# Kernel optimization log

Hardware: AMD Instinct MI355X
Metric: run time of the kernel (lower is better)

## Reference

```python
import jax, jax.numpy as jnp
import numpy as np

N = 80000      # nodes (spots)
D = 1000       # input_dim (genes)
E = 1280000    # edges (avg degree 16)
FH1, FH2 = 64, 16
GH1, GH2 = 64, 16
K = 10         # dec_cluster_n
ALPHA = 1.0
MASK = int(0.8 * N)
BN_EPS = 1e-3


def _xavier(key, shape):
    fan_in, fan_out = shape[0], shape[1]
    lim = jnp.sqrt(6.0 / (fan_in + fan_out))
    return jax.random.uniform(key, shape, jnp.float32, -lim, lim)


def setup_inputs() -> dict:
    key = jax.random.key(0)
    ks = jax.random.split(key, 32)
    x = jax.random.normal(ks[0], (N, D), jnp.float32)
    edge_rows = jax.random.randint(ks[1], (E,), 0, N, jnp.int32)
    edge_cols = jax.random.randint(ks[2], (E,), 0, N, jnp.int32)
    edge_vals = jax.random.uniform(ks[3], (E,), jnp.float32)
    mask_nodes = jax.random.permutation(ks[4], N)[:MASK].astype(jnp.int32)
    enc_mask_token = 0.02 * jax.random.normal(ks[5], (1, D), jnp.float32)
    # encoder L1: Linear + BatchNorm (eval: running stats)
    W1 = _xavier(ks[6], (D, FH1)); b1 = jnp.zeros((FH1,), jnp.float32)
    g1 = jnp.ones((FH1,), jnp.float32); be1 = jnp.zeros((FH1,), jnp.float32)
    rm1 = 0.1 * jax.random.normal(ks[7], (FH1,), jnp.float32)
    rv1 = 0.5 + jax.random.uniform(ks[8], (FH1,), jnp.float32)
    # encoder L2
    W2 = _xavier(ks[9], (FH1, FH2)); b2 = jnp.zeros((FH2,), jnp.float32)
    g2 = jnp.ones((FH2,), jnp.float32); be2 = jnp.zeros((FH2,), jnp.float32)
    rm2 = 0.1 * jax.random.normal(ks[10], (FH2,), jnp.float32)
    rv2 = 0.5 + jax.random.uniform(ks[11], (FH2,), jnp.float32)
    # GCN weights
    Wgc1 = _xavier(ks[12], (FH2, GH1))
    Wgc2 = _xavier(ks[13], (GH1, GH2))
    Wgc3 = _xavier(ks[14], (GH1, GH2))
    Wdec = _xavier(ks[15], (GH2 + FH2, D))
    cluster_layer = jax.random.normal(ks[16], (K, GH2 + FH2), jnp.float32) * jnp.sqrt(2.0 / (K + GH2 + FH2))
    return dict(x=x, edge_rows=edge_rows, edge_cols=edge_cols, edge_vals=edge_vals,
                mask_nodes=mask_nodes, enc_mask_token=enc_mask_token,
                W1=W1, b1=b1, g1=g1, be1=be1, rm1=rm1, rv1=rv1,
                W2=W2, b2=b2, g2=g2, be2=be2, rm2=rm2, rv2=rv2,
                Wgc1=Wgc1, Wgc2=Wgc2, Wgc3=Wgc3, Wdec=Wdec,
                cluster_layer=cluster_layer)


def _bn_eval(h, g, b, rm, rv):
    return (h - rm) * (g * jax.lax.rsqrt(rv + BN_EPS)) + b


def _spmm(rows, cols, vals, dense):
    # sparse adj [N,N] @ dense [N,F]
    return jax.ops.segment_sum(vals[:, None] * dense[cols], rows, num_segments=N)


def _l2norm(v):
    n = jnp.sqrt(jnp.sum(v * v, axis=-1, keepdims=True))
    return v / jnp.maximum(n, 1e-12)


def reference(x, edge_rows, edge_cols, edge_vals, mask_nodes, enc_mask_token,
              W1, b1, g1, be1, rm1, rv1, W2, b2, g2, be2, rm2, rv2,
              Wgc1, Wgc2, Wgc3, Wdec, cluster_layer):
    # encoding_mask_noise: add mask token to masked nodes (eval: dropout off)
    out_x = x.at[mask_nodes].add(enc_mask_token[0])
    # dense encoder (Linear -> BN(eval) -> ELU; dropout off)
    h = jax.nn.elu(_bn_eval(out_x @ W1 + b1, g1, be1, rm1, rv1))
    feat_x = jax.nn.elu(_bn_eval(h @ W2 + b2, g2, be2, rm2, rv2))
    # GCN layers: mm then spmm
    hidden1 = jax.nn.relu(_spmm(edge_rows, edge_cols, edge_vals, feat_x @ Wgc1))
    mu = _spmm(edge_rows, edge_cols, edge_vals, hidden1 @ Wgc2)
    logvar = _spmm(edge_rows, edge_cols, edge_vals, hidden1 @ Wgc3)
    gnn_z = mu  # eval-mode reparameterize
    z = jnp.concatenate([feat_x, gnn_z], axis=1)  # [N, 32]
    de_feat = _spmm(edge_rows, edge_cols, edge_vals, z @ Wdec)  # identity act
    # student-t cluster soft assignments
    d2 = jnp.sum(jnp.square(z[:, None, :] - cluster_layer[None, :, :]), axis=2)  # [N,K]
    q = 1.0 / (1.0 + d2 / ALPHA)
    q = q ** ((ALPHA + 1.0) / 2.0)
    q = q / jnp.sum(q, axis=1, keepdims=True)
    # sce loss on masked nodes
    x_init = out_x[mask_nodes]
    x_rec = de_feat[mask_nodes]
    loss = jnp.mean((1.0 - jnp.sum(_l2norm(x_rec) * _l2norm(x_init), axis=-1)) ** 3)
    return (z, mu, logvar, de_feat, q, feat_x, gnn_z, loss)
```

## Files before the change

kernel.cpp:

```cpp
#include <hip/hip_runtime.h>
#include <hip/hip_bf16.h>
#include <math.h>

#define Nn 80000
#define Dd 1000
#define Ee 1280000
#define MM 64000
#define NT 32

typedef __attribute__((ext_vector_type(8))) short bf16x8;
typedef __attribute__((ext_vector_type(4))) float f32x4;

__device__ inline unsigned short f2bf(float f){
  union { float f; unsigned u; } c; c.f = f;
  unsigned u = c.u;
  u += 0x7FFFu + ((u >> 16) & 1u);
  return (unsigned short)(u >> 16);
}
__device__ inline float bf2f(unsigned short s){
  return __uint_as_float(((unsigned)s) << 16);
}

__device__ __forceinline__ void gload16(const void* g, void* l){
  __builtin_amdgcn_global_load_lds(
      (const __attribute__((address_space(1))) void*)g,
      (__attribute__((address_space(3))) void*)l, 16, 0, 0);
}

__device__ __forceinline__ bf16x8 cvt8(f32x4 a, f32x4 b){
  union { __hip_bfloat162 h; unsigned u; } c0, c1, c2, c3;
  c0.h = __float22bfloat162_rn(make_float2(a.x, a.y));
  c1.h = __float22bfloat162_rn(make_float2(a.z, a.w));
  c2.h = __float22bfloat162_rn(make_float2(b.x, b.y));
  c3.h = __float22bfloat162_rn(make_float2(b.z, b.w));
  union { unsigned u[4]; bf16x8 v; } r;
  r.u[0] = c0.u; r.u[1] = c1.u; r.u[2] = c2.u; r.u[3] = c3.u;
  return r.v;
}

__global__ __launch_bounds__(256) void k_init(const float* __restrict__ W1,
    const float* __restrict__ Wdec, const float* __restrict__ token,
    unsigned short* __restrict__ Wim, unsigned short* __restrict__ WdT2,
    float* __restrict__ tw, int* __restrict__ flags, int* __restrict__ deg,
    float* __restrict__ loss)
{
  int i = blockIdx.x*256 + threadIdx.x;
  if (i < 131072){
    int t   = i >> 12;
    int rem = i & 4095;
    int c   = rem >> 5;
    int pos = rem & 31;
    int slot = pos >> 3;
    int j    = pos & 7;
    int u    = slot ^ (c & 3);
    int k    = t*32 + u*8 + j;
    float v = 0.f;
    if (c < 96 && k < Dd) v = (c < 64) ? W1[k*64 + c] : Wdec[(size_t)(c-64)*Dd + k];
    Wim[i] = f2bf(v);
  }
  unsigned t1 = (unsigned)(i - 131072);
  if (t1 < 32768u){
    int col = t1 >> 5, k = t1 & 31;
    WdT2[t1] = (col < Dd) ? f2bf(Wdec[(size_t)k*Dd + col]) : (unsigned short)0;
  }
  if (i < Nn){ flags[i] = 0; deg[i] = 0; }
  if (i == 0) *loss = 0.f;
  unsigned u3 = (unsigned)(i - 163840);
  if (u3 < 6208u){
    int j = u3 >> 6, l = u3 & 63;
    float s = 0.f;
    if (j < 64){ for (int k = l; k < Dd; k += 64) s += token[k]*W1[k*64 + j]; }
    else if (j < 96){ const float* wr = Wdec + (size_t)(j-64)*Dd;
                      for (int k = l; k < Dd; k += 64) s += token[k]*wr[k]; }
    else { for (int k = l; k < Dd; k += 64) s += token[k]*token[k]; }
    #pragma unroll
    for (int o = 32; o; o >>= 1) s += __shfl_down(s, o);
    if (l == 0) tw[j] = s;
  }
}

__global__ __launch_bounds__(256) void k_flags(const int* __restrict__ mask,
    int* __restrict__ flags)
{
  int i = blockIdx.x*256 + threadIdx.x;
  if (i < MM) flags[mask[i]] = 1;
}

__global__ __launch_bounds__(256, 3) void k_gemm1(
    const float* __restrict__ x, const unsigned short* __restrict__ Wim,
    const int* __restrict__ flags, const float* __restrict__ tw,
    const float* __restrict__ token,
    const float* __restrict__ b1, const float* __restrict__ g1,
    const float* __restrict__ be1, const float* __restrict__ rm1,
    const float* __restrict__ rv1, const float* __restrict__ W2,
    const float* __restrict__ b2, const float* __restrict__ g2,
    const float* __restrict__ be2, const float* __restrict__ rm2,
    const float* __restrict__ rv2, float* __restrict__ fx,
    float* __restrict__ wx, float* __restrict__ sii_node,
    const int* __restrict__ erow, const int* __restrict__ ecol,
    const float* __restrict__ evls, int* __restrict__ deg,
    int2* __restrict__ buck)
{
  __shared__ char smem[53248];
  if (blockIdx.x >= 625){
    int i = (blockIdx.x - 625)*256 + threadIdx.x;
    if (i < Ee){
      int r = erow[i];
      int s = atomicAdd(&deg[r], 1);
      if (s < 64){
        int2 pr; pr.x = ecol[i]; pr.y = __float_as_int(evls[i]);
        buck[((size_t)r << 6) + s] = pr;
      }
    }
    return;
  }
  float* tokL = (float*)(smem + 49152);
  const int tid  = threadIdx.x;
  const int lane = tid & 63;
  const int wave = tid >> 6;
  const int wm = wave >> 1, wn = wave & 1;
  const int l15 = lane & 15, kg = lane >> 4;
  const int swz = l15 & 7;
  const int row0 = blockIdx.x * 128;

  for (int i = tid; i < 1024; i += 256) tokL[i] = (i < Dd) ? token[i] : 0.f;
  __syncthreads();

  auto stage = [&](int t, char* Ab, char* Bb){
    int k0 = t*32;
    #pragma unroll
    for (int j = 0; j < 4; ++j){
      int s = (wave*4 + j)*64 + lane;
      int r = s >> 3, u = s & 7;
      int col = k0 + ((u ^ (r & 7)) << 2);
      if (col > 996) col = 996;
      gload16(x + (size_t)(row0 + r)*Dd + col, Ab + (wave*4 + j)*1024);
    }
    const char* wim = (const char*)Wim + (size_t)t*8192;
    #pragma unroll
    for (int j = 0; j < 2; ++j){
      int ch = wave*2 + j;
      gload16(wim + ch*1024 + lane*16, Bb + ch*1024);
    }
  };

  stage(0, smem,         smem + 32768);
  stage(1, smem + 16384, smem + 40960);

  const f32x4 zero4 = {0.f,0.f,0.f,0.f};
  f32x4 acc[4][3];
  #pragma unroll
  for (int i = 0; i < 4; ++i){ acc[i][0]=zero4; acc[i][1]=zero4; acc[i][2]=zero4; }
  float sx2[4] = {0.f,0.f,0.f,0.f};
  float sxt[4] = {0.f,0.f,0.f,0.f};

  #pragma unroll 2
  for (int t = 0; t < NT; ++t){
    if (t < NT-1) asm volatile("s_waitcnt vmcnt(6)" ::: "memory");
    else          asm volatile("s_waitcnt vmcnt(0)" ::: "memory");
    __builtin_amdgcn_s_barrier();
    __builtin_amdgcn_sched_barrier(0);

    const char* Ab = smem + (t&1)*16384;
    const char* Bb = smem + 32768 + (t&1)*8192;
    const int k0 = t*32;

    f32x4 tk0 = *(const f32x4*)(tokL + k0 + kg*8);
    f32x4 tk1 = *(const f32x4*)(tokL + k0 + kg*8 + 4);

    bf16x8 bfr[3];
    #pragma unroll
    for (int ni = 0; ni < 3; ++ni){
      int c = wn*48 + ni*16 + l15;
      bfr[ni] = *(const bf16x8*)(Bb + c*64 + ((kg ^ (c & 3)) << 4));
    }
    bool kv = (k0 + kg*8) <= 992;
    #pragma unroll
    for (int mi = 0; mi < 4; ++mi){
      int r = wm*64 + mi*16 + l15;
      f32x4 xa = *(const f32x4*)(Ab + r*128 + (((2*kg  ) ^ swz) << 4));
      f32x4 xb = *(const f32x4*)(Ab + r*128 + (((2*kg+1) ^ swz) << 4));
      if (wn == 0 && kv){
        sx2[mi] += xa.x*xa.x + xa.y*xa.y + xa.z*xa.z + xa.w*xa.w
                 + xb.x*xb.x + xb.y*xb.y + xb.z*xb.z + xb.w*xb.w;
        sxt[mi] += xa.x*tk0.x + xa.y*tk0.y + xa.z*tk0.z + xa.w*tk0.w
                 + xb.x*tk1.x + xb.y*tk1.y + xb.z*tk1.z + xb.w*tk1.w;
      }
      bf16x8 af = cvt8(xa, xb);
      acc[mi][0] = __builtin_amdgcn_mfma_f32_16x16x32_bf16(af, bfr[0], acc[mi][0], 0, 0, 0);
      acc[mi][1] = __builtin_amdgcn_mfma_f32_16x16x32_bf16(af, bfr[1], acc[mi][1], 0, 0, 0);
      acc[mi][2] = __builtin_amdgcn_mfma_f32_16x16x32_bf16(af, bfr[2], acc[mi][2], 0, 0, 0);
    }

    __builtin_amdgcn_sched_barrier(0);
    __builtin_amdgcn_s_barrier();
    if (t + 2 < NT)
      stage(t+2, smem + (t&1)*16384, smem + 32768 + (t&1)*8192);
  }

  float stt = tw[96];
  if (wn == 0){
    #pragma unroll
    for (int mi = 0; mi < 4; ++mi){
      float a2 = sx2[mi]; a2 += __shfl_xor(a2, 16); a2 += __shfl_xor(a2, 32);
      float at = sxt[mi]; at += __shfl_xor(at, 16); at += __shfl_xor(at, 32);
      if (lane < 16){
        int row = row0 + wm*64 + mi*16 + lane;
        float fl = flags[row] ? 1.f : 0.f;
        sii_node[row] = a2 + fl*(2.f*at + stt);
      }
    }
  }

  float flv[4][4];
  #pragma unroll
  for (int mi = 0; mi < 4; ++mi)
    #pragma unroll
    for (int r4 = 0; r4 < 4; ++r4)
      flv[mi][r4] = flags[row0 + wm*64 + mi*16 + (lane>>4)*4 + r4] ? 1.f : 0.f;

  float* Hs  = (float*)smem;
  float* W2s = (float*)(smem + 36864);
  for (int i = tid; i < 1024; i += 256) W2s[i] = W2[i];

  #pragma unroll
  for (int ni = 0; ni < 3; ++ni){
    int n = wn*48 + ni*16 + l15;
    float twn = tw[n];
    if (n < 64){
      float bb = b1[n], rmv = rm1[n];
      float scv = g1[n]*rsqrtf(rv1[n] + 1e-3f), bev = be1[n];
      #pragma unroll
      for (int mi = 0; mi < 4; ++mi){
        #pragma unroll
        for (int r4 = 0; r4 < 4; ++r4){
          int lrow = wm*64 + mi*16 + (lane>>4)*4 + r4;
          float v = (acc[mi][ni][r4] + flv[mi][r4]*twn + bb - rmv)*scv + bev;
          v = (v > 0.f) ? v : expm1f(v);
          Hs[lrow*66 + n] = v;
        }
      }
    } else {
      int j = n - 64;
      #pragma unroll
      for (int mi = 0; mi < 4; ++mi){
        #pragma unroll
        for (int r4 = 0; r4 < 4; ++r4){
          int lrow = wm*64 + mi*16 + (lane>>4)*4 + r4;
          wx[(size_t)(row0 + lrow)*32 + j] = acc[mi][ni][r4] + flv[mi][r4]*twn;
        }
      }
    }
  }
  __syncthreads();

  {
    int j = tid & 15;
    float pb = b2[j], prm = rm2[j];
    float psc = g2[j]*rsqrtf(rv2[j] + 1e-3f), pbe = be2[j];
    int rb = (tid >> 4) * 8;
    #pragma unroll
    for (int rr = 0; rr < 8; ++rr){
      int r = rb + rr;
      float a = pb;
      #pragma unroll
      for (int k = 0; k < 64; ++k) a += Hs[r*66 + k]*W2s[k*16 + j];
      float v = (a - prm)*psc + pbe;
      v = (v > 0.f) ? v : expm1f(v);
      fx[(size_t)(row0 + r)*16 + j] = v;
    }
  }
}

__global__ __launch_bounds__(256) void k_spmm16(const int* __restrict__ deg,
    const int2* __restrict__ buck, const float* __restrict__ in,
    float* __restrict__ out, const float* __restrict__ Wgc1,
    unsigned short* __restrict__ h1b)
{
  __shared__ float Ws[1024];
  for (int t = threadIdx.x; t < 1024; t += 256) Ws[t] = Wgc1[t];
  __syncthreads();
  int row = blockIdx.x*16 + (threadIdx.x >> 4);
  int l = threadIdx.x & 15;
  int d = deg[row]; if (d > 64) d = 64;
  const int2* bp = buck + ((size_t)row << 6);
  float acc = 0.f;
  for (int p = 0; p < d; ++p){
    int2 ce = bp[p];
    acc += __int_as_float(ce.y) * in[(size_t)ce.x*16 + l];
  }
  out[(size_t)row*16 + l] = acc;
  float h0=0.f, h1=0.f, h2=0.f, h3=0.f;
  #pragma unroll
  for (int k = 0; k < 16; ++k){
    float av = __shfl(acc, k, 16);
    const float* wp = &Ws[k*64 + l*4];
    h0 += av*wp[0]; h1 += av*wp[1]; h2 += av*wp[2]; h3 += av*wp[3];
  }
  ushort4 pk;
  pk.x = f2bf(fmaxf(h0, 0.f)); pk.y = f2bf(fmaxf(h1, 0.f));
  pk.z = f2bf(fmaxf(h2, 0.f)); pk.w = f2bf(fmaxf(h3, 0.f));
  *reinterpret_cast<ushort4*>(&h1b[(size_t)row*64 + l*4]) = pk;
}

__global__ __launch_bounds__(256) void k_gcn2(const int* __restrict__ deg,
    const int2* __restrict__ buck, const unsigned short* __restrict__ h1b,
    const float* __restrict__ Wgc2, const float* __restrict__ Wgc3,
    const float* __restrict__ fx, const float* __restrict__ cl,
    float* __restrict__ z, float* __restrict__ mu,
    float* __restrict__ lv, float* __restrict__ gz, float* __restrict__ q)
{
  __shared__ float ah[16][65];
  __shared__ float Ws[2048];
  __shared__ float cls[320];
  __shared__ float zs[16][33];
  __shared__ float qv[16][10];
  int t = threadIdx.x;
  for (int i = t; i < 1024; i += 256){ Ws[i] = Wgc2[i]; Ws[1024 + i] = Wgc3[i]; }
  for (int i = t; i < 320; i += 256) cls[i] = cl[i];
  const int wave = t >> 6, lane = t & 63;
  const int row0 = blockIdx.x*16;
  #pragma unroll
  for (int rr = 0; rr < 4; ++rr){
    int lr = wave*4 + rr;
    int row = row0 + lr;
    int d = deg[row]; if (d > 64) d = 64;
    const int2* bp = buck + ((size_t)row << 6);
    float acc = 0.f;
    for (int p = 0; p < d; ++p){
      int2 ce = bp[p];
      acc += __int_as_float(ce.y) * bf2f(h1b[(size_t)ce.x*64 + lane]);
    }
    ah[lr][lane] = acc;
  }
  __syncthreads();
  {
    int r = t >> 4, j = t & 15;
    const float* ar = ah[r];
    float m = 0.f, l = 0.f;
    #pragma unroll 16
    for (int k = 0; k < 64; ++k){
      float a = ar[k];
      m += a*Ws[k*16 + j];
      l += a*Ws[1024 + k*16 + j];
    }
    size_t grow = (size_t)(row0 + r);
    mu[grow*16 + j] = m;
    gz[grow*16 + j] = m;
    z[grow*32 + 16 + j] = m;
    zs[r][16 + j] = m;
    lv[grow*16 + j] = l;
    float v = fx[grow*16 + j];
    z[grow*32 + j] = v;
    zs[r][j] = v;
  }
  __syncthreads();
  if (t < 160){
    int r = t / 10, c = t - r*10;
    float d2 = 0.f;
    #pragma unroll
    for (int k = 0; k < 32; ++k){ float d = zs[r][k] - cls[c*32 + k]; d2 += d*d; }
    qv[r][c] = 1.f/(1.f + d2);
  }
  __syncthreads();
  if (t < 160){
    int r = t / 10, c = t - r*10;
    float ss = 0.f;
    #pragma unroll
    for (int cc = 0; cc < 10; ++cc) ss += qv[r][cc];
    q[(size_t)(row0 + r)*10 + c] = qv[r][c]/ss;
  }
}

__global__ __launch_bounds__(256) void k_dec(const float* __restrict__ afx,
    const float* __restrict__ mu, const int* __restrict__ deg,
    const int2* __restrict__ buck, const unsigned short* __restrict__ WdT2,
    const float* __restrict__ wx, const float* __restrict__ sii_node,
    const int* __restrict__ flags, float* __restrict__ de,
    float* __restrict__ loss)
{
  __shared__ float stg[4][16][68];
  __shared__ float amuL[64][17];
  __shared__ float bsum[4];
  const int tid  = threadIdx.x;
  const int lane = tid & 63;
  const int wave = tid >> 6;
  const int base = blockIdx.x*64;

  {
    int l = tid & 15, rg = tid >> 4;
    #pragma unroll
    for (int pass = 0; pass < 4; ++pass){
      int lr = pass*16 + rg;
      int row = base + lr;
      int d = deg[row]; if (d > 64) d = 64;
      const int2* bp = buck + ((size_t)row << 6);
      float acc = 0.f;
      for (int p = 0; p < d; ++p){
        int2 ce = bp[p];
        acc += __int_as_float(ce.y) * mu[(size_t)ce.x*16 + l];
      }
      amuL[lr][l] = acc;
    }
  }
  __syncthreads();

  const int r0 = base + wave*16;
  const int kg = lane >> 4;
  const int l15 = lane & 15;
  const int row = r0 + l15;
  f32x4 a0, a1;
  if (kg < 2){
    const float* asrc = afx + (size_t)row*16 + kg*8;
    a0 = *reinterpret_cast<const f32x4*>(asrc);
    a1 = *reinterpret_cast<const f32x4*>(asrc + 4);
  } else {
    const float* asrc = &amuL[wave*16 + l15][(kg-2)*8];
    a0 = *reinterpret_cast<const f32x4*>(asrc);
    a1 = *reinterpret_cast<const f32x4*>(asrc + 4);
  }
  bf16x8 af = cvt8(a0, a1);
  const float* wsrc = wx + (size_t)row*32 + kg*8;
  f32x4 w0 = *reinterpret_cast<const f32x4*>(wsrc);
  f32x4 w1 = *reinterpret_cast<const f32x4*>(wsrc + 4);
  float sri = a0.x*w0.x + a0.y*w0.y + a0.z*w0.z + a0.w*w0.w
            + a1.x*w1.x + a1.y*w1.y + a1.z*w1.z + a1.w*w1.w;

  const f32x4 zero4 = {0.f,0.f,0.f,0.f};
  float sq = 0.f;
  float (*S)[68] = stg[wave];
  const int srow = lane >> 4;
  const int scol = l15*4;

  for (int g = 0; g < 16; ++g){
    int c0 = g*64;
    #pragma unroll
    for (int j = 0; j < 4; ++j){
      int cb = c0 + j*16;
      bf16x8 bf = *reinterpret_cast<const bf16x8*>(&WdT2[(size_t)(cb + l15)*32 + kg*8]);
      f32x4 d = __builtin_amdgcn_mfma_f32_16x16x32_bf16(bf, af, zero4, 0, 0, 0);
      sq += d[0]*d[0] + d[1]*d[1] + d[2]*d[2] + d[3]*d[3];
      *reinterpret_cast<f32x4*>(&S[l15][j*16 + kg*4]) = d;
    }
    asm volatile("s_waitcnt lgkmcnt(0)" ::: "memory");
    __builtin_amdgcn_sched_barrier(0);
    #pragma unroll
    for (int sub = 0; sub < 4; ++sub){
      int lr = sub*4 + srow;
      int cc = c0 + scol;
      if (cc < Dd){
        f32x4 v = *reinterpret_cast<const f32x4*>(&S[lr][scol]);
        *reinterpret_cast<f32x4*>(&de[(size_t)(r0 + lr)*Dd + cc]) = v;
      }
    }
    __builtin_amdgcn_sched_barrier(0);
    asm volatile("s_waitcnt lgkmcnt(0)" ::: "memory");
  }
  sq  += __shfl_xor(sq, 16);  sq  += __shfl_xor(sq, 32);
  sri += __shfl_xor(sri, 16); sri += __shfl_xor(sri, 32);
  float tval = 0.f;
  if (kg == 0){
    float nr = fmaxf(sqrtf(sq), 1e-12f);
    float ni = fmaxf(sqrtf(sii_node[row]), 1e-12f);
    float tt = 1.f - sri/(nr*ni);
    tval = flags[row] ? tt*tt*tt : 0.f;
  }
  #pragma unroll
  for (int o = 1; o < 16; o <<= 1) tval += __shfl_xor(tval, o);
  if (lane == 0) bsum[wave] = tval;
  __syncthreads();
  if (tid == 0)
    atomicAdd(loss, (bsum[0] + bsum[1] + bsum[2] + bsum[3]) * (1.f/MM));
}

extern "C" void kernel_launch(void* const* d_in, const int* in_sizes, int n_in,
                              void* d_out, int out_size, void* d_ws, size_t ws_size,
                              hipStream_t stream)
{
  const float* x     = (const float*)d_in[0];
  const int*   erow  = (const int*)  d_in[1];
  const int*   ecol  = (const int*)  d_in[2];
  const float* evls  = (const float*)d_in[3];
  const int*   mask  = (const int*)  d_in[4];
  const float* token = (const float*)d_in[5];
  const float* W1  = (const float*)d_in[6];
  const float* b1  = (const float*)d_in[7];
  const float* g1  = (const float*)d_in[8];
  const float* be1 = (const float*)d_in[9];
  const float* rm1 = (const float*)d_in[10];
  const float* rv1 = (const float*)d_in[11];
  const float* W2  = (const float*)d_in[12];
  const float* b2  = (const float*)d_in[13];
  const float* g2  = (const float*)d_in[14];
  const float* be2 = (const float*)d_in[15];
  const float* rm2 = (const float*)d_in[16];
  const float* rv2 = (const float*)d_in[17];
  const float* Wgc1= (const float*)d_in[18];
  const float* Wgc2= (const float*)d_in[19];
  const float* Wgc3= (const float*)d_in[20];
  const float* Wdec= (const float*)d_in[21];
  const float* clus= (const float*)d_in[22];

  float* out = (float*)d_out;
  float* oz  = out;
  float* omu = out + (size_t)Nn*32;
  float* olv = omu + (size_t)Nn*16;
  float* ode = olv + (size_t)Nn*16;
  float* oq  = ode + (size_t)Nn*1000;
  float* ofx = oq  + (size_t)Nn*10;
  float* ogz = ofx + (size_t)Nn*16;
  float* olo = ogz + (size_t)Nn*16;

  char* w = (char*)d_ws;
  unsigned short* Wim  = (unsigned short*)w; w += (size_t)262144;
  unsigned short* WdT2 = (unsigned short*)w; w += (size_t)65536;
  float* tw    = (float*)w; w += 512;
  int* flags   = (int*)w;   w += (size_t)Nn*4;
  int* deg     = (int*)w;   w += (size_t)Nn*4;
  int2* buck   = (int2*)w;  w += (size_t)Nn*64*8;
  float* afx   = (float*)w; w += (size_t)Nn*16*4;
  unsigned short* h1b = (unsigned short*)w; w += (size_t)Nn*64*2;
  float* wx    = (float*)w; w += (size_t)Nn*32*4;
  float* sii   = (float*)w; w += (size_t)Nn*4;

  k_init<<<dim3(665), dim3(256), 0, stream>>>(W1, Wdec, token, Wim, WdT2, tw,
      flags, deg, olo);
  k_flags<<<dim3((MM+255)/256), dim3(256), 0, stream>>>(mask, flags);
  k_gemm1<<<dim3(5625), dim3(256), 0, stream>>>(x, Wim, flags, tw, token,
      b1, g1, be1, rm1, rv1, W2, b2, g2, be2, rm2, rv2, ofx, wx, sii,
      erow, ecol, evls, deg, buck);
  k_spmm16<<<dim3(Nn/16), dim3(256), 0, stream>>>(deg, buck, ofx, afx, Wgc1, h1b);
  k_gcn2<<<dim3(Nn/16), dim3(256), 0, stream>>>(deg, buck, h1b, Wgc2, Wgc3,
      ofx, clus, oz, omu, olv, ogz, oq);
  k_dec<<<dim3(Nn/64), dim3(256), 0, stream>>>(afx, omu, deg, buck, WdT2,
      wx, sii, flags, ode, olo);
}
```

Baseline: 489.7 us.

## Stage x through registers as bf16 in LDS to shrink shared memory for occupancy

After: 485.8 us, median of 2. No clear change (-0.8%).

```diff
diff --git a/kernel.cpp b/kernel.cpp
--- a/kernel.cpp
+++ b/kernel.cpp
@@ -86,7 +86,7 @@
   if (i < MM) flags[mask[i]] = 1;
 }
 
-__global__ __launch_bounds__(256, 3) void k_gemm1(
+__global__ __launch_bounds__(256, 4) void k_gemm1(
     const float* __restrict__ x, const unsigned short* __restrict__ Wim,
     const int* __restrict__ flags, const float* __restrict__ tw,
     const float* __restrict__ token,
@@ -101,7 +101,7 @@
     const float* __restrict__ evls, int* __restrict__ deg,
     int2* __restrict__ buck)
 {
-  __shared__ char smem[53248];
+  __shared__ char smem[37888];
   if (blockIdx.x >= 625){
     int i = (blockIdx.x - 625)*256 + threadIdx.x;
     if (i < Ee){
@@ -114,38 +114,36 @@
     }
     return;
   }
-  float* tokL = (float*)(smem + 49152);
+  unsigned short* As = (unsigned short*)smem;
+  float* tokL = (float*)(smem + 24576);
   const int tid  = threadIdx.x;
   const int lane = tid & 63;
   const int wave = tid >> 6;
   const int wm = wave >> 1, wn = wave & 1;
   const int l15 = lane & 15, kg = lane >> 4;
-  const int swz = l15 & 7;
   const int row0 = blockIdx.x * 128;
 
+  const int rtid = tid >> 3;
+  const int kq   = (tid & 7) * 4;
+  const int wu   = (kq >> 3) ^ (rtid & 3) ^ ((rtid >> 2) & 3);
+  const int wofs = rtid*32 + wu*8 + (kq & 4);
+
+  const float* xbase = x + (size_t)row0 * Dd;
+  f32x4 ra[4];
+
   for (int i = tid; i < 1024; i += 256) tokL[i] = (i < Dd) ? token[i] : 0.f;
-  __syncthreads();
-
-  auto stage = [&](int t, char* Ab, char* Bb){
-    int k0 = t*32;
-    #pragma unroll
-    for (int j = 0; j < 4; ++j){
-      int s = (wave*4 + j)*64 + lane;
-      int r = s >> 3, u = s & 7;
-      int col = k0 + ((u ^ (r & 7)) << 2);
-      if (col > 996) col = 996;
-      gload16(x + (size_t)(row0 + r)*Dd + col, Ab + (wave*4 + j)*1024);
-    }
-    const char* wim = (const char*)Wim + (size_t)t*8192;
-    #pragma unroll
-    for (int j = 0; j < 2; ++j){
-      int ch = wave*2 + j;
-      gload16(wim + ch*1024 + lane*16, Bb + ch*1024);
-    }
-  };
-
-  stage(0, smem,         smem + 32768);
-  stage(1, smem + 16384, smem + 40960);
+
+  {
+    int col = kq;
+    #pragma unroll
+    for (int j = 0; j < 4; ++j)
+      ra[j] = *(const f32x4*)(xbase + (size_t)(j*32 + rtid)*Dd + col);
+    const char* wim = (const char*)Wim;
+    gload16(wim + (wave*2  )*1024 + lane*16, smem + 8192 + (wave*2  )*1024);
+    gload16(wim + (wave*2+1)*1024 + lane*16, smem + 8192 + (wave*2+1)*1024);
+  }
+  asm volatile("s_waitcnt lgkmcnt(0)" ::: "memory");
+  __builtin_amdgcn_s_barrier();
 
   const f32x4 zero4 = {0.f,0.f,0.f,0.f};
   f32x4 acc[4][3];
@@ -156,17 +154,42 @@
 
   #pragma unroll 2
   for (int t = 0; t < NT; ++t){
-    if (t < NT-1) asm volatile("s_waitcnt vmcnt(6)" ::: "memory");
-    else          asm volatile("s_waitcnt vmcnt(0)" ::: "memory");
+    const char* Bb = smem + 8192 + (t&1)*8192;
+    const int k0 = t*32;
+    const bool kok = (t < NT-1) || (kq <= 4);
+    f32x4 tok4 = *(const f32x4*)(tokL + k0 + kq);
+
+    #pragma unroll
+    for (int j = 0; j < 4; ++j){
+      f32x4 v = ra[j];
+      if (kok){
+        sx2[j] += v.x*v.x + v.y*v.y + v.z*v.z + v.w*v.w;
+        sxt[j] += v.x*tok4.x + v.y*tok4.y + v.z*tok4.z + v.w*tok4.w;
+      }
+      union { __hip_bfloat162 h; unsigned u; } c0, c1;
+      c0.h = __float22bfloat162_rn(make_float2(v.x, v.y));
+      c1.h = __float22bfloat162_rn(make_float2(v.z, v.w));
+      uint2 pk; pk.x = c0.u; pk.y = c1.u;
+      *reinterpret_cast<uint2*>(&As[j*1024 + wofs]) = pk;
+    }
+
+    if (t + 1 < NT){
+      int col = k0 + 32 + kq; if (col > 996) col = 996;
+      #pragma unroll
+      for (int j = 0; j < 4; ++j)
+        ra[j] = *(const f32x4*)(xbase + (size_t)(j*32 + rtid)*Dd + col);
+      const char* wim = (const char*)Wim + (size_t)(t+1)*8192;
+      char* Bn = smem + 8192 + ((t+1)&1)*8192;
+      gload16(wim + (wave*2  )*1024 + lane*16, Bn + (wave*2  )*1024);
+      gload16(wim + (wave*2+1)*1024 + lane*16, Bn + (wave*2+1)*1024);
+      asm volatile("s_waitcnt lgkmcnt(0)" ::: "memory");
+      asm volatile("s_waitcnt vmcnt(6)" ::: "memory");
+    } else {
+      asm volatile("s_waitcnt lgkmcnt(0)" ::: "memory");
+      asm volatile("s_waitcnt vmcnt(0)" ::: "memory");
+    }
     __builtin_amdgcn_s_barrier();
     __builtin_amdgcn_sched_barrier(0);
-
-    const char* Ab = smem + (t&1)*16384;
-    const char* Bb = smem + 32768 + (t&1)*8192;
-    const int k0 = t*32;
-
-    f32x4 tk0 = *(const f32x4*)(tokL + k0 + kg*8);
-    f32x4 tk1 = *(const f32x4*)(tokL + k0 + kg*8 + 4);
 
     bf16x8 bfr[3];
     #pragma unroll
@@ -174,41 +197,30 @@
       int c = wn*48 + ni*16 + l15;
       bfr[ni] = *(const bf16x8*)(Bb + c*64 + ((kg ^ (c & 3)) << 4));
     }
-    bool kv = (k0 + kg*8) <= 992;
+    const int ru = (kg ^ (l15 & 3) ^ ((l15 >> 2) & 3)) << 4;
     #pragma unroll
     for (int mi = 0; mi < 4; ++mi){
       int r = wm*64 + mi*16 + l15;
-      f32x4 xa = *(const f32x4*)(Ab + r*128 + (((2*kg  ) ^ swz) << 4));
-      f32x4 xb = *(const f32x4*)(Ab + r*128 + (((2*kg+1) ^ swz) << 4));
-      if (wn == 0 && kv){
-        sx2[mi] += xa.x*xa.x + xa.y*xa.y + xa.z*xa.z + xa.w*xa.w
-                 + xb.x*xb.x + xb.y*xb.y + xb.z*xb.z + xb.w*xb.w;
-        sxt[mi] += xa.x*tk0.x + xa.y*tk0.y + xa.z*tk0.z + xa.w*tk0.w
-                 + xb.x*tk1.x + xb.y*tk1.y + xb.z*tk1.z + xb.w*tk1.w;
-      }
-      bf16x8 af = cvt8(xa, xb);
+      bf16x8 af = *(const bf16x8*)((const char*)As + r*64 + ru);
       acc[mi][0] = __builtin_amdgcn_mfma_f32_16x16x32_bf16(af, bfr[0], acc[mi][0], 0, 0, 0);
       acc[mi][1] = __builtin_amdgcn_mfma_f32_16x16x32_bf16(af, bfr[1], acc[mi][1], 0, 0, 0);
       acc[mi][2] = __builtin_amdgcn_mfma_f32_16x16x32_bf16(af, bfr[2], acc[mi][2], 0, 0, 0);
     }
-
     __builtin_amdgcn_sched_barrier(0);
     __builtin_amdgcn_s_barrier();
-    if (t + 2 < NT)
-      stage(t+2, smem + (t&1)*16384, smem + 32768 + (t&1)*8192);
   }
 
   float stt = tw[96];
-  if (wn == 0){
-    #pragma unroll
-    for (int mi = 0; mi < 4; ++mi){
-      float a2 = sx2[mi]; a2 += __shfl_xor(a2, 16); a2 += __shfl_xor(a2, 32);
-      float at = sxt[mi]; at += __shfl_xor(at, 16); at += __shfl_xor(at, 32);
-      if (lane < 16){
-        int row = row0 + wm*64 + mi*16 + lane;
-        float fl = flags[row] ? 1.f : 0.f;
-        sii_node[row] = a2 + fl*(2.f*at + stt);
-      }
+  #pragma unroll
+  for (int j = 0; j < 4; ++j){
+    float a2 = sx2[j], at = sxt[j];
+    a2 += __shfl_xor(a2, 1); at += __shfl_xor(at, 1);
+    a2 += __shfl_xor(a2, 2); at += __shfl_xor(at, 2);
+    a2 += __shfl_xor(a2, 4); at += __shfl_xor(at, 4);
+    if ((tid & 7) == 0){
+      int row = row0 + j*32 + rtid;
+      float fl = flags[row] ? 1.f : 0.f;
+      sii_node[row] = a2 + fl*(2.f*at + stt);
     }
   }
 
@@ -220,7 +232,7 @@
       flv[mi][r4] = flags[row0 + wm*64 + mi*16 + (lane>>4)*4 + r4] ? 1.f : 0.f;
 
   float* Hs  = (float*)smem;
-  float* W2s = (float*)(smem + 36864);
+  float* W2s = (float*)(smem + 33792);
   for (int i = tid; i < 1024; i += 256) W2s[i] = W2[i];
 
   #pragma unroll
```
